# Kernel tuning notes

Hardware: AMD Instinct MI355X
Metric: run time of the kernel (lower is better)

The kernel has to match this reference:

```python
import jax, jax.numpy as jnp
import numpy as np

B, S, D, H, L = 16, 1024, 512, 8, 3
NUM_Q, NUM_C, TOTAL_RES = 10000, 300, 2


def setup_inputs() -> dict:
    k = jax.random.split(jax.random.key(0), 20)
    n = lambda i, s, sc=0.02: jax.random.normal(k[i], s, jnp.float32) * sc
    z = lambda: jnp.zeros((D,), jnp.float32)
    o = lambda: jnp.ones((D,), jnp.float32)
    return {
        'in_ex': jax.random.randint(k[0], (B, S), 0, NUM_Q),
        'in_cat': jax.random.randint(k[1], (B, S), 0, NUM_C),
        'in_res': jax.random.randint(k[2], (B, S), 0, 2),
        'in_pos': n(3, (B, S, D)),
        'en_out': n(4, (B, S, D)),
        'E_res': n(5, (TOTAL_RES + 1, D)),
        'E_ex': n(6, (2 * NUM_Q + 1, D)),
        'E_cat': n(7, (2 * NUM_C + 1, D)),
        'g1': o(), 'be1': z(), 'g2': o(), 'be2': z(), 'g3': o(), 'be3': z(),
        'Wq1': n(8, (D, D)), 'bq1': z(), 'Wk1': n(9, (D, D)), 'bk1': z(),
        'Wv1': n(10, (D, D)), 'bv1': z(), 'Wo1': n(11, (D, D)), 'bo1': z(),
        'Wq2': n(12, (D, D)), 'bq2': z(), 'Wk2': n(13, (D, D)), 'bk2': z(),
        'Wv2': n(14, (D, D)), 'bv2': z(), 'Wo2': n(15, (D, D)), 'bo2': z(),
        'fW1': n(16, (D, D)), 'fb1': z(), 'fW2': n(17, (D, D)), 'fb2': z(),
    }


def layer_norm(x, g, b, eps=1e-5):
    m = x.mean(-1, keepdims=True)
    v = ((x - m) ** 2).mean(-1, keepdims=True)
    return (x - m) / jnp.sqrt(v + eps) * g + b


def pyr_attn(q_in, kv_in, Wq, bq, Wk, bk, Wv, bv, Wo, bo):
    # q_in, kv_in: (S, B, D) as in nn.MultiheadAttention convention
    Sq, Bq, Dm = q_in.shape
    dh = Dm // H
    heads = lambda x: x.reshape(x.shape[0], Bq, H, dh).transpose(1, 2, 0, 3)  # (B,H,S,dh)
    qh = heads(q_in @ Wq + bq)
    kh = heads(kv_in @ Wk + bk)
    vh = heads(kv_in @ Wv + bv)
    Skv = kv_in.shape[0]
    i = jnp.arange(Sq)[:, None]
    Ks, Vs, Ms = [], [], []
    for l in range(L):  # pyramid levels: keys/values avg-pooled by 2**l
        f = 2 ** l
        nb = Skv // f
        Ks.append(kh[:, :, :nb * f].reshape(Bq, H, nb, f, dh).mean(3))
        Vs.append(vh[:, :, :nb * f].reshape(Bq, H, nb, f, dh).mean(3))
        # causal: query i may attend pooled block j only if the block ends at or before i
        Ms.append(i >= (jnp.arange(nb)[None, :] + 1) * f - 1)
    K = jnp.concatenate(Ks, 2)
    V = jnp.concatenate(Vs, 2)
    M = jnp.concatenate(Ms, 1)  # (Sq, K_total) multi-level causal mask
    sc = jnp.einsum('bhqd,bhkd->bhqk', qh, K) / np.sqrt(dh).astype(np.float32)
    sc = jnp.where(M[None, None], sc, -1e9)
    a = jax.nn.softmax(sc, -1)
    out = jnp.einsum('bhqk,bhkd->bhqd', a, V)
    return out.transpose(2, 0, 1, 3).reshape(Sq, Bq, Dm) @ Wo + bo


def reference(in_ex, in_cat, in_res, in_pos, en_out, E_res, E_ex, E_cat,
              g1, be1, g2, be2, g3, be3,
              Wq1, bq1, Wk1, bk1, Wv1, bv1, Wo1, bo1,
              Wq2, bq2, Wk2, bk2, Wv2, bv2, Wo2, bo2,
              fW1, fb1, fW2, fb2):
    # embedding sum (first_block=True)
    out = E_res[in_res] + E_ex[in_ex + NUM_Q * in_res] + E_cat[in_cat + NUM_C * in_res] + in_pos
    out = out.transpose(1, 0, 2)  # (S, B, D)
    out = layer_norm(out, g1, be1)
    out = out + pyr_attn(out, out, Wq1, bq1, Wk1, bk1, Wv1, bv1, Wo1, bo1)
    en = layer_norm(en_out.transpose(1, 0, 2), g2, be2)
    out = out + pyr_attn(out, en, Wq2, bq2, Wk2, bk2, Wv2, bv2, Wo2, bo2)
    out = out.transpose(1, 0, 2)  # (B, S, D)
    out = layer_norm(out, g3, be3)
    out = out + (jax.nn.relu(out @ fW1 + fb1) @ fW2 + fb2)
    return out
```

## Files before the change

kernel.cpp:

```cpp
#include <hip/hip_runtime.h>


#define BB 16
#define SS 1024
#define DD 512
#define HH 8
#define DH 64
#define KTOT 1792
#define NROW (BB*SS)
#define KSW 80

typedef unsigned short u16;
typedef __attribute__((ext_vector_type(8))) u16 u16x8;
typedef __attribute__((ext_vector_type(4))) u16 u16x4;
typedef __attribute__((ext_vector_type(8))) short s16x8;
typedef __attribute__((ext_vector_type(4))) float f32x4;

__device__ __forceinline__ float b2f(u16 u) {
    return __uint_as_float(((unsigned int)u) << 16);
}
__device__ __forceinline__ u16 f2b(float f) {
    unsigned int u = __float_as_uint(f);
    return (u16)((u + 0x7FFF + ((u >> 16) & 1)) >> 16);
}
__device__ __forceinline__ s16x8 u2s8(u16x8 u) {
    union { u16x8 u; s16x8 s; } x; x.u = u; return x.s;
}
__device__ __forceinline__ f32x4 mfma16(s16x8 a, s16x8 b, f32x4 c) {
    return __builtin_amdgcn_mfma_f32_16x16x32_bf16(a, b, c, 0, 0, 0);
}
__device__ __forceinline__ float wave_sum(float v) {
    #pragma unroll
    for (int m = 1; m < 64; m <<= 1) v += __shfl_xor(v, m, 64);
    return v;
}
__device__ __forceinline__ float exp2a(float x) {
    float r;
    asm("v_exp_f32 %0, %1" : "=v"(r) : "v"(x));
    return r;
}
__device__ __forceinline__ unsigned int cvtpk(float a, float b) {
    unsigned int r;
    asm("v_cvt_pk_bf16_f32 %0, %1, %2" : "=v"(r) : "v"(a), "v"(b));
    return r;
}
__device__ __forceinline__ void gl16(const void* g, void* l) {
    __builtin_amdgcn_global_load_lds(
        (const __attribute__((address_space(1))) void*)(unsigned long long)g,
        (__attribute__((address_space(3))) void*)(unsigned int)(unsigned long long)l,
        16, 0, 0);
}

__global__ __launch_bounds__(256) void embed_ln_k(
    const int* __restrict__ in_ex, const int* __restrict__ in_cat,
    const int* __restrict__ in_res, const float* __restrict__ in_pos,
    const float* __restrict__ E_res, const float* __restrict__ E_ex,
    const float* __restrict__ E_cat, const float* __restrict__ g,
    const float* __restrict__ be, float* __restrict__ out)
{
    int wave = threadIdx.x >> 6, lane = threadIdx.x & 63;
    int row = blockIdx.x * 4 + wave;
    int res = in_res[row];
    int ex  = in_ex[row] + 10000 * res;
    int cat = in_cat[row] + 300 * res;
    int d0 = lane * 8;
    const float* pr = &E_res[(size_t)res * DD + d0];
    const float* pe = &E_ex[(size_t)ex * DD + d0];
    const float* pc = &E_cat[(size_t)cat * DD + d0];
    const float* pp = &in_pos[(size_t)row * DD + d0];
    float x[8]; float s = 0.f;
    #pragma unroll
    for (int j = 0; j < 8; j++) { x[j] = pr[j] + pe[j] + pc[j] + pp[j]; s += x[j]; }
    s = wave_sum(s);
    float mean = s * (1.0f / DD);
    float vs = 0.f;
    #pragma unroll
    for (int j = 0; j < 8; j++) { float d = x[j] - mean; vs += d * d; }
    vs = wave_sum(vs);
    float rstd = rsqrtf(vs * (1.0f / DD) + 1e-5f);
    #pragma unroll
    for (int j = 0; j < 8; j++)
        out[(size_t)row * DD + d0 + j] = (x[j] - mean) * rstd * g[d0 + j] + be[d0 + j];
}

template<bool OUTB>
__global__ __launch_bounds__(256) void ln_k(
    const float* __restrict__ x, const float* __restrict__ g,
    const float* __restrict__ be, void* __restrict__ outv)
{
    int wave = threadIdx.x >> 6, lane = threadIdx.x & 63;
    int row = blockIdx.x * 4 + wave;
    int d0 = lane * 8;
    const float* px = &x[(size_t)row * DD + d0];
    float xv[8]; float s = 0.f;
    #pragma unroll
    for (int j = 0; j < 8; j++) { xv[j] = px[j]; s += xv[j]; }
    s = wave_sum(s);
    float mean = s * (1.0f / DD);
    float vs = 0.f;
    #pragma unroll
    for (int j = 0; j < 8; j++) { float d = xv[j] - mean; vs += d * d; }
    vs = wave_sum(vs);
    float rstd = rsqrtf(vs * (1.0f / DD) + 1e-5f);
    #pragma unroll
    for (int j = 0; j < 8; j++) {
        float v = (xv[j] - mean) * rstd * g[d0 + j] + be[d0 + j];
        if (OUTB) ((u16*)outv)[(size_t)row * DD + d0 + j] = f2b(v);
        else      ((float*)outv)[(size_t)row * DD + d0 + j] = v;
    }
}

struct W10 { const float* p[10]; };
__global__ __launch_bounds__(256) void transpose_all_k(W10 wp, u16* __restrict__ dst)
{
    __shared__ __align__(16) u16 T[64 * 72];
    int w = blockIdx.z;
    const float* src = wp.p[w];
    u16* d = dst + (size_t)w * 262144;
    int tk = blockIdx.x;
    int tn = blockIdx.y;
    int tid = threadIdx.x;
    {
        int r = tid >> 4;
        int c4 = (tid & 15) * 4;
        #pragma unroll
        for (int it = 0; it < 4; it++) {
            int kr = it * 16 + r;
            const float* s4 = &src[(size_t)(tk * 64 + kr) * 512 + tn * 64 + c4];
            f32x4 v = *(const f32x4*)s4;
            *(unsigned int*)&T[kr * 72 + c4]     = cvtpk(v[0], v[1]);
            *(unsigned int*)&T[kr * 72 + c4 + 2] = cvtpk(v[2], v[3]);
        }
    }
    __syncthreads();
    {
        int nn = tid >> 2;
        int k16 = (tid & 3) * 16;
        u16x8 a, b;
        #pragma unroll
        for (int j = 0; j < 8; j++) {
            a[j] = T[(k16 + j) * 72 + nn];
            b[j] = T[(k16 + 8 + j) * 72 + nn];
        }
        u16* o = &d[(size_t)(tn * 64 + nn) * 512 + tk * 64 + k16];
        *(u16x8*)&o[0] = a;
        *(u16x8*)&o[8] = b;
    }
}

__global__ __launch_bounds__(256) void pool_vt_k(const u16* __restrict__ Vp, u16* __restrict__ VPt)
{
    __shared__ __align__(16) u16 T[64 * 72];
    int tid = threadIdx.x;
    int st = blockIdx.x;
    int h  = blockIdx.y;
    int b  = blockIdx.z;
    int s0 = st * 64;
    {
        const u16* src = &Vp[((size_t)(b * SS + s0)) * DD + h * DH];
        #pragma unroll
        for (int it = 0; it < 2; it++) {
            int idx = it * 256 + tid;
            int row = idx >> 3, unit = idx & 7;
            *(u16x8*)&T[row * 72 + unit * 8] =
                *(const u16x8*)&src[(size_t)row * DD + unit * 8];
        }
    }
    __syncthreads();
    int d = tid & 63, g = tid >> 6;
    size_t obase = ((size_t)(b * HH + h) * DH + d) * KTOT;
    #pragma unroll
    for (int gg = 0; gg < 2; gg++) {
        int grp = g * 2 + gg;
        u16x8 v;
        #pragma unroll
        for (int j = 0; j < 8; j++) v[j] = T[(grp * 8 + j) * 72 + d];
        *(u16x8*)&VPt[obase + s0 + grp * 8] = v;
    }
    {
        u16x8 v;
        #pragma unroll
        for (int j = 0; j < 8; j++) {
            int sl = g * 8 + j;
            float a = b2f(T[(2 * sl) * 72 + d]) + b2f(T[(2 * sl + 1) * 72 + d]);
            v[j] = f2b(a * 0.5f);
        }
        *(u16x8*)&VPt[obase + 1024 + st * 32 + g * 8] = v;
    }
    {
        u16x4 v;
        #pragma unroll
        for (int j = 0; j < 4; j++) {
            int s2 = g * 4 + j;
            float a = 0.f;
            #pragma unroll
            for (int i = 0; i < 4; i++) a += b2f(T[(4 * s2 + i) * 72 + d]);
            v[j] = f2b(a * 0.25f);
        }
        *(u16x4*)&VPt[obase + 1536 + st * 16 + g * 4] = v;
    }
}

template<bool AF32, bool RELU, bool RES, bool OUTB, bool KLAY>
__global__ __launch_bounds__(256) void gemm_k(
    const void* __restrict__ Av, const u16* __restrict__ Wt,
    const float* __restrict__ bias, const float* __restrict__ resid,
    void* __restrict__ Cv, int M, int K, float oscale)
{
    const int N = 512;
    constexpr int ASW = AF32 ? 40 : 32;
    __shared__ __align__(16) u16 As[2][128 * ASW];
    __shared__ __align__(16) u16 Bs[2][128 * 32];
    int tid = threadIdx.x;
    int wave = tid >> 6, lane = tid & 63;
    int quad = lane >> 4, l16 = lane & 15;
    int m0 = blockIdx.y * 128, n0 = blockIdx.x * 128;
    int wm = (wave >> 1) * 64, wn = (wave & 1) * 64;
    int r = tid >> 1, cg = (tid & 1) * 16;
    int grow = wave * 16 + (lane >> 2);
    int gk = (lane & 3) * 8;
    const float* Af = (const float*)Av;
    const u16*  Ab = (const u16*)Av;
    f32x4 acc[4][4];
    #pragma unroll
    for (int i = 0; i < 4; i++)
        #pragma unroll
        for (int j = 0; j < 4; j++)
            #pragma unroll
            for (int rr = 0; rr < 4; rr++) acc[i][j][rr] = 0.f;

    const int NT = K >> 5;
    f32x4 s0, s1, s2, s3;

    #define ISSUE_B(t, buf) { int k0_ = (t) << 5; \
        gl16(&Wt[(size_t)(n0 + grow) * 512 + k0_ + gk],      &Bs[buf][grow * 32 + gk]); \
        gl16(&Wt[(size_t)(n0 + 64 + grow) * 512 + k0_ + gk], &Bs[buf][(64 + grow) * 32 + gk]); }
    #define ISSUE_A16(t, buf) { int k0_ = (t) << 5; \
        gl16(&Ab[(size_t)(m0 + grow) * K + k0_ + gk],      &As[buf][grow * 32 + gk]); \
        gl16(&Ab[(size_t)(m0 + 64 + grow) * K + k0_ + gk], &As[buf][(64 + grow) * 32 + gk]); }
    #define LOAD_A32(t) { const float* src_ = &Af[(size_t)(m0 + r) * K + ((t) << 5) + cg]; \
        s0 = *(const f32x4*)&src_[0];  s1 = *(const f32x4*)&src_[4]; \
        s2 = *(const f32x4*)&src_[8];  s3 = *(const f32x4*)&src_[12]; }
    #define WRITE_A32(buf) { union { unsigned int w[4]; u16x8 v; } L_, H_; \
        L_.w[0] = cvtpk(s0[0], s0[1]); L_.w[1] = cvtpk(s0[2], s0[3]); \
        L_.w[2] = cvtpk(s1[0], s1[1]); L_.w[3] = cvtpk(s1[2], s1[3]); \
        H_.w[0] = cvtpk(s2[0], s2[1]); H_.w[1] = cvtpk(s2[2], s2[3]); \
        H_.w[2] = cvtpk(s3[0], s3[1]); H_.w[3] = cvtpk(s3[2], s3[3]); \
        *(u16x8*)&As[buf][r * ASW + cg]     = L_.v; \
        *(u16x8*)&As[buf][r * ASW + cg + 8] = H_.v; }

    if (AF32) { LOAD_A32(0); WRITE_A32(0); }
    else      { ISSUE_A16(0, 0); }
    ISSUE_B(0, 0);
    __syncthreads();

    for (int t = 0; t < NT; ++t) {
        int cur = t & 1, nxt = cur ^ 1;
        if (t + 1 < NT) {
            if (AF32) { LOAD_A32(t + 1); }
            else      { ISSUE_A16(t + 1, nxt); }
            ISSUE_B(t + 1, nxt);
        }
        s16x8 af[4], bfr[4];
        #pragma unroll
        for (int i = 0; i < 4; i++)
            af[i] = u2s8(*(const u16x8*)&As[cur][(wm + i * 16 + l16) * ASW + quad * 8]);
        #pragma unroll
        for (int j = 0; j < 4; j++)
            bfr[j] = u2s8(*(const u16x8*)&Bs[cur][(wn + j * 16 + l16) * 32 + quad * 8]);
        #pragma unroll
        for (int i = 0; i < 4; i++)
            #pragma unroll
            for (int j = 0; j < 4; j++)
                acc[i][j] = mfma16(af[i], bfr[j], acc[i][j]);
        if (AF32 && t + 1 < NT) { WRITE_A32(nxt); }
        __syncthreads();
    }
    #undef ISSUE_B
    #undef ISSUE_A16
    #undef LOAD_A32
    #undef WRITE_A32

    #pragma unroll
    for (int j = 0; j < 4; j++) {
        int col = n0 + wn + j * 16 + l16;
        float bv = bias[col];
        #pragma unroll
        for (int i = 0; i < 4; i++) {
            int rowb = m0 + wm + i * 16 + quad * 4;
            if (KLAY) {
                float vv[4];
                #pragma unroll
                for (int rr = 0; rr < 4; rr++) vv[rr] = acc[i][j][rr] + bv;
                int b_ = rowb >> 10, s_ = rowb & 1023;
                size_t bh = (size_t)(b_ * HH + (col >> 6)) * KTOT;
                int dd = col & 63;
                u16* C16 = (u16*)Cv;
                #pragma unroll
                for (int rr = 0; rr < 4; rr++)
                    C16[(bh + s_ + rr) * DH + dd] = f2b(vv[rr]);
                C16[(bh + 1024 + (s_ >> 1)) * DH + dd]     = f2b((vv[0] + vv[1]) * 0.5f);
                C16[(bh + 1024 + (s_ >> 1) + 1) * DH + dd] = f2b((vv[2] + vv[3]) * 0.5f);
                C16[(bh + 1536 + (s_ >> 2)) * DH + dd]     = f2b((vv[0] + vv[1] + vv[2] + vv[3]) * 0.25f);
            } else {
                #pragma unroll
                for (int rr = 0; rr < 4; rr++) {
                    float v = (acc[i][j][rr] + bv) * oscale;
                    if (RELU) v = fmaxf(v, 0.f);
                    int row = rowb + rr;
                    if (RES) v += resid[(size_t)row * N + col];
                    if (OUTB) ((u16*)Cv)[(size_t)row * N + col] = f2b(v);
                    else      ((float*)Cv)[(size_t)row * N + col] = v;
                }
            }
        }
    }
}

__global__ __launch_bounds__(256, 4) void attn_k(
    const u16* __restrict__ Qp, const u16* __restrict__ KP,
    const u16* __restrict__ VPt, u16* __restrict__ Hout)
{
    __shared__ __align__(16) u16 Ksh[2][64 * KSW];
    __shared__ __align__(16) u16 Vsh[2][64 * KSW];
    int tid = threadIdx.x;
    int wave = tid >> 6, lane = tid & 63;
    int quad = lane >> 4, l16 = lane & 15;
    int id = blockIdx.x;
    int h = id & 7;
    int inner = id >> 3;
    int x = inner & 7, b = inner >> 3;

    int wg = x * 4 + wave;
    int tiles[2] = { wg, 63 - wg };

    const u16* Kb = KP  + ((size_t)(b * HH + h)) * KTOT * DH;
    const u16* Vt = VPt + ((size_t)(b * HH + h)) * DH * KTOT;

    s16x8 qa[2][2];
    f32x4 o[2][4];
    float lrun[2];
    int q0a[2];
    #pragma unroll
    for (int c = 0; c < 2; c++) {
        int q0 = tiles[c] * 16;
        q0a[c] = q0;
        lrun[c] = 0.f;
        const u16* qrow = Qp + ((size_t)(b * SS + q0 + l16)) * DD + h * DH;
        qa[c][0] = u2s8(*(const u16x8*)&qrow[quad * 8]);
        qa[c][1] = u2s8(*(const u16x8*)&qrow[32 + quad * 8]);
        #pragma unroll
        for (int j = 0; j < 4; j++)
            #pragma unroll
            for (int rr = 0; rr < 4; rr++) o[c][j][rr] = 0.f;
    }

    int row0 = 8 * (l16 >> 2) + (l16 & 3);

    int u0 = tid, u1 = 256 + tid;
    int kr0 = u0 >> 3, ku0 = (u0 & 7) * 8;
    int kr1 = u1 >> 3, ku1 = (u1 & 7) * 8;

    u16x8 kreg0 = *(const u16x8*)&Kb[(size_t)u0 * 8];
    u16x8 kreg1 = *(const u16x8*)&Kb[(size_t)u1 * 8];
    u16x8 vreg0 = *(const u16x8*)&Vt[(size_t)kr0 * KTOT + ku0];
    u16x8 vreg1 = *(const u16x8*)&Vt[(size_t)kr1 * KTOT + ku1];
    *(u16x8*)&Ksh[0][kr0 * KSW + ku0] = kreg0;
    *(u16x8*)&Ksh[0][kr1 * KSW + ku1] = kreg1;
    *(u16x8*)&Vsh[0][kr0 * KSW + ku0] = vreg0;
    *(u16x8*)&Vsh[0][kr1 * KSW + ku1] = vreg1;
    __syncthreads();

    for (int ch = 0; ch < 28; ch++) {
        int cur = ch & 1;
        int kbase = ch * 64;
        int lv = (ch < 16) ? 0 : (ch < 24) ? 1 : 2;
        if (ch + 1 < 28) {
            int nb = (ch + 1) * 64;
            kreg0 = *(const u16x8*)&Kb[(size_t)nb * DH + u0 * 8];
            kreg1 = *(const u16x8*)&Kb[(size_t)nb * DH + u1 * 8];
            vreg0 = *(const u16x8*)&Vt[(size_t)kr0 * KTOT + nb + ku0];
            vreg1 = *(const u16x8*)&Vt[(size_t)kr1 * KTOT + nb + ku1];
        }

        int efirst = (lv == 0) ? kbase
                   : (lv == 1) ? 2 * (kbase - 1024) + 1
                               : 4 * (kbase - 1536) + 3;
        int elast  = (lv == 0) ? kbase + 63
                   : (lv == 1) ? 2 * (kbase + 63 - 1024) + 1
                               : 4 * (kbase + 63 - 1536) + 3;
        bool act[2];
        #pragma unroll
        for (int c = 0; c < 2; c++) act[c] = (efirst <= q0a[c] + 15);

        if (act[0] | act[1]) {
            s16x8 fA[4], fB[4];
            #pragma unroll
            for (int t = 0; t < 4; t++) {
                const int toff = (t & 1) * 4 + (t >> 1) * 32;
                const u16* kr = &Ksh[cur][(row0 + toff) * KSW];
                fA[t] = u2s8(*(const u16x8*)&kr[quad * 8]);
                fB[t] = u2s8(*(const u16x8*)&kr[32 + quad * 8]);
            }
            s16x8 pfa[2], pfb[2];
            #pragma unroll
            for (int c = 0; c < 2; c++) {
                if (!act[c]) continue;
                f32x4 zt[4];
                __builtin_amdgcn_s_setprio(1);
                #pragma unroll
                for (int t = 0; t < 4; t++) {
                    f32x4 z;
                    #pragma unroll
                    for (int rr = 0; rr < 4; rr++) z[rr] = 0.f;
                    z = mfma16(fA[t], qa[c][0], z);
                    zt[t] = mfma16(fB[t], qa[c][1], z);
                }
                __builtin_amdgcn_s_setprio(0);

                if (elast > q0a[c]) {
                    int q = q0a[c] + l16;
                    int kmaxv = (lv == 0) ? q - kbase
                              : (lv == 1) ? ((q - 1) >> 1) - (kbase - 1024)
                                          : ((q - 3) >> 2) - (kbase - 1536);
                    int thrb = kmaxv - 8 * quad;
                    #pragma unroll
                    for (int t = 0; t < 4; t++) {
                        int thr = thrb - ((t & 1) * 4 + (t >> 1) * 32);
                        #pragma unroll
                        for (int rr = 0; rr < 4; rr++)
                            if (rr > thr) zt[t][rr] = -1e30f;
                    }
                }

                float p[4][4]; float ps0 = 0.f, ps1 = 0.f;
                #pragma unroll
                for (int t = 0; t < 4; t++)
                    #pragma unroll
                    for (int rr = 0; rr < 4; rr++) {
                        p[t][rr] = exp2a(zt[t][rr]);
                        if (t & 1) ps1 += p[t][rr]; else ps0 += p[t][rr];
                    }
                float ps = ps0 + ps1;
                ps += __shfl_xor(ps, 16, 64);
                ps += __shfl_xor(ps, 32, 64);
                lrun[c] += ps;

                union { unsigned int w[4]; u16x8 v; } U0, U1;
                U0.w[0] = cvtpk(p[0][0], p[0][1]); U0.w[1] = cvtpk(p[0][2], p[0][3]);
                U0.w[2] = cvtpk(p[1][0], p[1][1]); U0.w[3] = cvtpk(p[1][2], p[1][3]);
                U1.w[0] = cvtpk(p[2][0], p[2][1]); U1.w[1] = cvtpk(p[2][2], p[2][3]);
                U1.w[2] = cvtpk(p[3][0], p[3][1]); U1.w[3] = cvtpk(p[3][2], p[3][3]);
                pfa[c] = u2s8(U0.v); pfb[c] = u2s8(U1.v);
            }

            s16x8 vA[4], vB[4];
            #pragma unroll
            for (int j = 0; j < 4; j++) {
                const u16* vr = &Vsh[cur][(j * 16 + l16) * KSW];
                vA[j] = u2s8(*(const u16x8*)&vr[quad * 8]);
                vB[j] = u2s8(*(const u16x8*)&vr[32 + quad * 8]);
            }
            __builtin_amdgcn_s_setprio(1);
            #pragma unroll
            for (int c = 0; c < 2; c++) {
                if (!act[c]) continue;
                #pragma unroll
                for (int j = 0; j < 4; j++) {
                    o[c][j] = mfma16(pfa[c], vA[j], o[c][j]);
                    o[c][j] = mfma16(pfb[c], vB[j], o[c][j]);
                }
            }
            __builtin_amdgcn_s_setprio(0);
        }

        if (ch + 1 < 28) {
            int nxt = cur ^ 1;
            *(u16x8*)&Ksh[nxt][kr0 * KSW + ku0] = kreg0;
            *(u16x8*)&Ksh[nxt][kr1 * KSW + ku1] = kreg1;
            *(u16x8*)&Vsh[nxt][kr0 * KSW + ku0] = vreg0;
            *(u16x8*)&Vsh[nxt][kr1 * KSW + ku1] = vreg1;
        }
        __syncthreads();
    }

    #pragma unroll
    for (int c = 0; c < 2; c++) {
        float il = 1.0f / lrun[c];
        float ilr[4];
        #pragma unroll
        for (int rr = 0; rr < 4; rr++) ilr[rr] = __shfl(il, quad * 4 + rr, 64);
        #pragma unroll
        for (int rr = 0; rr < 4; rr++) {
            int q = q0a[c] + quad * 4 + rr;
            #pragma unroll
            for (int j = 0; j < 4; j++)
                Hout[((size_t)(b * SS + q)) * DD + h * DH + j * 16 + l16] = f2b(o[c][j][rr] * ilr[rr]);
        }
    }
}

extern "C" void kernel_launch(void* const* d_in, const int* in_sizes, int n_in,
                              void* d_out, int out_size, void* d_ws, size_t ws_size,
                              hipStream_t stream)
{
    (void)in_sizes; (void)n_in; (void)out_size; (void)ws_size;
    const int* in_ex  = (const int*)d_in[0];
    const int* in_cat = (const int*)d_in[1];
    const int* in_res = (const int*)d_in[2];
    const float* in_pos = (const float*)d_in[3];
    const float* en_out = (const float*)d_in[4];
    const float* E_res  = (const float*)d_in[5];
    const float* E_ex   = (const float*)d_in[6];
    const float* E_cat  = (const float*)d_in[7];
    const float* g1 = (const float*)d_in[8],  *be1 = (const float*)d_in[9];
    const float* g2 = (const float*)d_in[10], *be2 = (const float*)d_in[11];
    const float* g3 = (const float*)d_in[12], *be3 = (const float*)d_in[13];
    const float* Wq1 = (const float*)d_in[14], *bq1 = (const float*)d_in[15];
    const float* Wk1 = (const float*)d_in[16], *bk1 = (const float*)d_in[17];
    const float* Wv1 = (const float*)d_in[18], *bv1 = (const float*)d_in[19];
    const float* Wo1 = (const float*)d_in[20], *bo1 = (const float*)d_in[21];
    const float* Wq2 = (const float*)d_in[22], *bq2 = (const float*)d_in[23];
    const float* Wk2 = (const float*)d_in[24], *bk2 = (const float*)d_in[25];
    const float* Wv2 = (const float*)d_in[26], *bv2 = (const float*)d_in[27];
    const float* Wo2 = (const float*)d_in[28], *bo2 = (const float*)d_in[29];
    const float* fW1 = (const float*)d_in[30], *fb1 = (const float*)d_in[31];
    const float* fW2 = (const float*)d_in[32], *fb2 = (const float*)d_in[33];

    char* ws = (char*)d_ws;
    const size_t U = (size_t)NROW * DD * 2;
    float* x1 = (float*)(ws);
    u16* qb   = (u16*)(ws + 2 * U);
    u16* vb   = (u16*)(ws + 3 * U);
    u16* hb   = (u16*)(ws + 4 * U);
    u16* kp   = (u16*)(ws + 5 * U);
    u16* vpt  = (u16*)(ws + 5 * U + 7 * U / 4);
    u16* wt   = (u16*)(ws + 8 * U + U / 2);
    float* x2 = (float*)d_out;
    u16* en = (u16*)(ws);
    float* x3 = x1;
    float* x4 = (float*)(ws + 5 * U);
    u16* ff1 = hb;

    W10 wp;
    const float* wsrc[10] = {Wq1, Wk1, Wv1, Wo1, Wq2, Wk2, Wv2, Wo2, fW1, fW2};
    for (int i = 0; i < 10; i++) wp.p[i] = wsrc[i];
    transpose_all_k<<<dim3(8, 8, 10), 256, 0, stream>>>(wp, wt);
    u16* tWq1 = wt,            *tWk1 = wt + 262144,   *tWv1 = wt + 2*262144, *tWo1 = wt + 3*262144;
    u16* tWq2 = wt + 4*262144, *tWk2 = wt + 5*262144, *tWv2 = wt + 6*262144, *tWo2 = wt + 7*262144;
    u16* tF1  = wt + 8*262144, *tF2  = wt + 9*262144;

    dim3 ggrid(4, 128);
    dim3 vtgrid(16, 8, 16);
    const float QSC = 0.18033688f;

    embed_ln_k<<<4096, 256, 0, stream>>>(in_ex, in_cat, in_res, in_pos,
                                         E_res, E_ex, E_cat, g1, be1, x1);

    gemm_k<true,false,false,true,false><<<ggrid, 256, 0, stream>>>(x1, tWq1, bq1, nullptr, qb, NROW, 512, QSC);
    gemm_k<true,false,false,true,true ><<<ggrid, 256, 0, stream>>>(x1, tWk1, bk1, nullptr, kp, NROW, 512, 1.0f);
    gemm_k<true,false,false,true,false><<<ggrid, 256, 0, stream>>>(x1, tWv1, bv1, nullptr, vb, NROW, 512, 1.0f);
    pool_vt_k<<<vtgrid, 256, 0, stream>>>(vb, vpt);
    attn_k<<<1024, 256, 0, stream>>>(qb, kp, vpt, hb);
    gemm_k<false,false,true,false,false><<<ggrid, 256, 0, stream>>>(hb, tWo1, bo1, x1, x2, NROW, 512, 1.0f);

    ln_k<true><<<4096, 256, 0, stream>>>(en_out, g2, be2, en);
    gemm_k<true,false,false,true,false><<<ggrid, 256, 0, stream>>>(x2, tWq2, bq2, nullptr, qb, NROW, 512, QSC);
    gemm_k<false,false,false,true,true ><<<ggrid, 256, 0, stream>>>(en, tWk2, bk2, nullptr, kp, NROW, 512, 1.0f);
    gemm_k<false,false,false,true,false><<<ggrid, 256, 0, stream>>>(en, tWv2, bv2, nullptr, vb, NROW, 512, 1.0f);
    pool_vt_k<<<vtgrid, 256, 0, stream>>>(vb, vpt);
    attn_k<<<1024, 256, 0, stream>>>(qb, kp, vpt, hb);
    gemm_k<false,false,true,false,false><<<ggrid, 256, 0, stream>>>(hb, tWo2, bo2, x2, x3, NROW, 512, 1.0f);

    ln_k<false><<<4096, 256, 0, stream>>>(x3, g3, be3, x4);
    gemm_k<true,true,false,true,false><<<ggrid, 256, 0, stream>>>(x4, tF1, fb1, nullptr, ff1, NROW, 512, 1.0f);
    gemm_k<false,false,true,false,false><<<ggrid, 256, 0, stream>>>(ff1, tF2, fb2, x4, (float*)d_out, NROW, 512, 1.0f);
}
```

Baseline: 709.7 us.

## Fuse QKV and KV projection GEMMs into one launch; restructure attention to 8 waves

Adds a fused GEMM kernel that picks one of up to three weight/bias/output sets from blockIdx.x, so the Q/K/V projections (and the cross-attention K/V projections) each run as a single launch sharing the A-matrix stream. Separately, the attention kernel is reworked to use 512 threads with one 16-row query tile per wave instead of two tiles per wave. It also drops the double-buffered shared K/V tiles in favour of a single buffer with two barriers per chunk. This cuts launch count and gives the GPU more concurrent work per launch, at the cost of losing the causal load-balancing tile pairing (wave*8+x gives uneven work across waves) and shared-memory double buffering.

```diff
diff --git a/kernel.cpp b/kernel.cpp
--- a/kernel.cpp
+++ b/kernel.cpp
@@ -276,10 +276,6 @@
         if (AF32 && t + 1 < NT) { WRITE_A32(nxt); }
         __syncthreads();
     }
-    #undef ISSUE_B
-    #undef ISSUE_A16
-    #undef LOAD_A32
-    #undef WRITE_A32
 
     #pragma unroll
     for (int j = 0; j < 4; j++) {
@@ -315,14 +311,148 @@
             }
         }
     }
-}
-
-__global__ __launch_bounds__(256, 4) void attn_k(
+    #undef ISSUE_B
+    #undef ISSUE_A16
+    #undef LOAD_A32
+    #undef WRITE_A32
+}
+
+struct FArgs {
+    const u16* W[3]; const float* bias[3]; void* C[3];
+    float osc[3]; int mode[3];
+};
+template<bool AF32>
+__global__ __launch_bounds__(256) void fused_gemm_k(
+    const void* __restrict__ Av, FArgs fa, int M, int K)
+{
+    constexpr int ASW = AF32 ? 40 : 32;
+    __shared__ __align__(16) u16 As[2][128 * ASW];
+    __shared__ __align__(16) u16 Bs[2][128 * 32];
+    int gsel = blockIdx.x >> 2;
+    int n0 = (blockIdx.x & 3) * 128;
+    const u16* Wt = fa.W[gsel];
+    const float* bias = fa.bias[gsel];
+    void* Cv = fa.C[gsel];
+    float oscale = fa.osc[gsel];
+    int mode = fa.mode[gsel];
+
+    int tid = threadIdx.x;
+    int wave = tid >> 6, lane = tid & 63;
+    int quad = lane >> 4, l16 = lane & 15;
+    int m0 = blockIdx.y * 128;
+    int wm = (wave >> 1) * 64, wn = (wave & 1) * 64;
+    int r = tid >> 1, cg = (tid & 1) * 16;
+    int grow = wave * 16 + (lane >> 2);
+    int gk = (lane & 3) * 8;
+    const float* Af = (const float*)Av;
+    const u16*  Ab = (const u16*)Av;
+    f32x4 acc[4][4];
+    #pragma unroll
+    for (int i = 0; i < 4; i++)
+        #pragma unroll
+        for (int j = 0; j < 4; j++)
+            #pragma unroll
+            for (int rr = 0; rr < 4; rr++) acc[i][j][rr] = 0.f;
+
+    const int NT = K >> 5;
+    f32x4 s0, s1, s2, s3;
+
+    #define ISSUE_B(t, buf) { int k0_ = (t) << 5; \
+        gl16(&Wt[(size_t)(n0 + grow) * 512 + k0_ + gk],      &Bs[buf][grow * 32 + gk]); \
+        gl16(&Wt[(size_t)(n0 + 64 + grow) * 512 + k0_ + gk], &Bs[buf][(64 + grow) * 32 + gk]); }
+    #define ISSUE_A16(t, buf) { int k0_ = (t) << 5; \
+        gl16(&Ab[(size_t)(m0 + grow) * K + k0_ + gk],      &As[buf][grow * 32 + gk]); \
+        gl16(&Ab[(size_t)(m0 + 64 + grow) * K + k0_ + gk], &As[buf][(64 + grow) * 32 + gk]); }
+    #define LOAD_A32(t) { const float* src_ = &Af[(size_t)(m0 + r) * K + ((t) << 5) + cg]; \
+        s0 = *(const f32x4*)&src_[0];  s1 = *(const f32x4*)&src_[4]; \
+        s2 = *(const f32x4*)&src_[8];  s3 = *(const f32x4*)&src_[12]; }
+    #define WRITE_A32(buf) { union { unsigned int w[4]; u16x8 v; } L_, H_; \
+        L_.w[0] = cvtpk(s0[0], s0[1]); L_.w[1] = cvtpk(s0[2], s0[3]); \
+        L_.w[2] = cvtpk(s1[0], s1[1]); L_.w[3] = cvtpk(s1[2], s1[3]); \
+        H_.w[0] = cvtpk(s2[0], s2[1]); H_.w[1] = cvtpk(s2[2], s2[3]); \
+        H_.w[2] = cvtpk(s3[0], s3[1]); H_.w[3] = cvtpk(s3[2], s3[3]); \
+        *(u16x8*)&As[buf][r * ASW + cg]     = L_.v; \
+        *(u16x8*)&As[buf][r * ASW + cg + 8] = H_.v; }
+
+    if (AF32) { LOAD_A32(0); WRITE_A32(0); }
+    else      { ISSUE_A16(0, 0); }
+    ISSUE_B(0, 0);
+    __syncthreads();
+
+    for (int t = 0; t < NT; ++t) {
+        int cur = t & 1, nxt = cur ^ 1;
+        if (t + 1 < NT) {
+            if (AF32) { LOAD_A32(t + 1); }
+            else      { ISSUE_A16(t + 1, nxt); }
+            ISSUE_B(t + 1, nxt);
+        }
+        s16x8 af[4], bfr[4];
+        #pragma unroll
+        for (int i = 0; i < 4; i++)
+            af[i] = u2s8(*(const u16x8*)&As[cur][(wm + i * 16 + l16) * ASW + quad * 8]);
+        #pragma unroll
+        for (int j = 0; j < 4; j++)
+            bfr[j] = u2s8(*(const u16x8*)&Bs[cur][(wn + j * 16 + l16) * 32 + quad * 8]);
+        #pragma unroll
+        for (int i = 0; i < 4; i++)
+            #pragma unroll
+            for (int j = 0; j < 4; j++)
+                acc[i][j] = mfma16(af[i], bfr[j], acc[i][j]);
+        if (AF32 && t + 1 < NT) { WRITE_A32(nxt); }
+        __syncthreads();
+    }
+    #undef ISSUE_B
+    #undef ISSUE_A16
+    #undef LOAD_A32
+    #undef WRITE_A32
+
+    if (mode == 1) {
+        #pragma unroll
+        for (int j = 0; j < 4; j++) {
+            int col = n0 + wn + j * 16 + l16;
+            float bv = bias[col];
+            #pragma unroll
+            for (int i = 0; i < 4; i++) {
+                int rowb = m0 + wm + i * 16 + quad * 4;
+                float vv[4];
+                #pragma unroll
+                for (int rr = 0; rr < 4; rr++) vv[rr] = acc[i][j][rr] + bv;
+                int b_ = rowb >> 10, s_ = rowb & 1023;
+                size_t bh = (size_t)(b_ * HH + (col >> 6)) * KTOT;
+                int dd = col & 63;
+                u16* C16 = (u16*)Cv;
+                #pragma unroll
+                for (int rr = 0; rr < 4; rr++)
+                    C16[(bh + s_ + rr) * DH + dd] = f2b(vv[rr]);
+                C16[(bh + 1024 + (s_ >> 1)) * DH + dd]     = f2b((vv[0] + vv[1]) * 0.5f);
+                C16[(bh + 1024 + (s_ >> 1) + 1) * DH + dd] = f2b((vv[2] + vv[3]) * 0.5f);
+                C16[(bh + 1536 + (s_ >> 2)) * DH + dd]     = f2b((vv[0] + vv[1] + vv[2] + vv[3]) * 0.25f);
+            }
+        }
+    } else {
+        #pragma unroll
+        for (int j = 0; j < 4; j++) {
+            int col = n0 + wn + j * 16 + l16;
+            float bv = bias[col];
+            #pragma unroll
+            for (int i = 0; i < 4; i++) {
+                int rowb = m0 + wm + i * 16 + quad * 4;
+                #pragma unroll
+                for (int rr = 0; rr < 4; rr++) {
+                    float v = (acc[i][j][rr] + bv) * oscale;
+                    ((u16*)Cv)[(size_t)(rowb + rr) * 512 + col] = f2b(v);
+                }
+            }
+        }
+    }
+}
+
+__global__ __launch_bounds__(512) void attn_k(
     const u16* __restrict__ Qp, const u16* __restrict__ KP,
     const u16* __restrict__ VPt, u16* __restrict__ Hout)
 {
-    __shared__ __align__(16) u16 Ksh[2][64 * KSW];
-    __shared__ __align__(16) u16 Vsh[2][64 * KSW];
+    __shared__ __align__(16) u16 Ksh[64 * KSW];
+    __shared__ __align__(16) u16 Vsh[64 * KSW];
     int tid = threadIdx.x;
     int wave = tid >> 6, lane = tid & 63;
     int quad = lane >> 4, l16 = lane & 15;
@@ -331,171 +461,125 @@
     int inner = id >> 3;
     int x = inner & 7, b = inner >> 3;
 
-    int wg = x * 4 + wave;
-    int tiles[2] = { wg, 63 - wg };
+    int tile = wave * 8 + x;
+    int q0 = tile * 16;
 
     const u16* Kb = KP  + ((size_t)(b * HH + h)) * KTOT * DH;
     const u16* Vt = VPt + ((size_t)(b * HH + h)) * DH * KTOT;
 
-    s16x8 qa[2][2];
-    f32x4 o[2][4];
-    float lrun[2];
-    int q0a[2];
-    #pragma unroll
-    for (int c = 0; c < 2; c++) {
-        int q0 = tiles[c] * 16;
-        q0a[c] = q0;
-        lrun[c] = 0.f;
+    s16x8 qa0, qa1;
+    f32x4 o[4];
+    float lrun = 0.f;
+    {
         const u16* qrow = Qp + ((size_t)(b * SS + q0 + l16)) * DD + h * DH;
-        qa[c][0] = u2s8(*(const u16x8*)&qrow[quad * 8]);
-        qa[c][1] = u2s8(*(const u16x8*)&qrow[32 + quad * 8]);
+        qa0 = u2s8(*(const u16x8*)&qrow[quad * 8]);
+        qa1 = u2s8(*(const u16x8*)&qrow[32 + quad * 8]);
         #pragma unroll
         for (int j = 0; j < 4; j++)
             #pragma unroll
-            for (int rr = 0; rr < 4; rr++) o[c][j][rr] = 0.f;
+            for (int rr = 0; rr < 4; rr++) o[j][rr] = 0.f;
     }
 
     int row0 = 8 * (l16 >> 2) + (l16 & 3);
 
-    int u0 = tid, u1 = 256 + tid;
-    int kr0 = u0 >> 3, ku0 = (u0 & 7) * 8;
-    int kr1 = u1 >> 3, ku1 = (u1 & 7) * 8;
-
-    u16x8 kreg0 = *(const u16x8*)&Kb[(size_t)u0 * 8];
-    u16x8 kreg1 = *(const u16x8*)&Kb[(size_t)u1 * 8];
-    u16x8 vreg0 = *(const u16x8*)&Vt[(size_t)kr0 * KTOT + ku0];
-    u16x8 vreg1 = *(const u16x8*)&Vt[(size_t)kr1 * KTOT + ku1];
-    *(u16x8*)&Ksh[0][kr0 * KSW + ku0] = kreg0;
-    *(u16x8*)&Ksh[0][kr1 * KSW + ku1] = kreg1;
-    *(u16x8*)&Vsh[0][kr0 * KSW + ku0] = vreg0;
-    *(u16x8*)&Vsh[0][kr1 * KSW + ku1] = vreg1;
-    __syncthreads();
+    int srow = tid >> 3, sunit = tid & 7;
+    u16x8 kreg = *(const u16x8*)&Kb[(size_t)tid * 8];
+    u16x8 vreg = *(const u16x8*)&Vt[(size_t)srow * KTOT + sunit * 8];
 
     for (int ch = 0; ch < 28; ch++) {
-        int cur = ch & 1;
         int kbase = ch * 64;
         int lv = (ch < 16) ? 0 : (ch < 24) ? 1 : 2;
+        __syncthreads();
+        *(u16x8*)&Ksh[srow * KSW + sunit * 8] = kreg;
+        *(u16x8*)&Vsh[srow * KSW + sunit * 8] = vreg;
+        __syncthreads();
         if (ch + 1 < 28) {
             int nb = (ch + 1) * 64;
-            kreg0 = *(const u16x8*)&Kb[(size_t)nb * DH + u0 * 8];
-            kreg1 = *(const u16x8*)&Kb[(size_t)nb * DH + u1 * 8];
-            vreg0 = *(const u16x8*)&Vt[(size_t)kr0 * KTOT + nb + ku0];
-            vreg1 = *(const u16x8*)&Vt[(size_t)kr1 * KTOT + nb + ku1];
+            kreg = *(const u16x8*)&Kb[(size_t)nb * DH + tid * 8];
+            vreg = *(const u16x8*)&Vt[(size_t)srow * KTOT + nb + sunit * 8];
         }
 
         int efirst = (lv == 0) ? kbase
                    : (lv == 1) ? 2 * (kbase - 1024) + 1
                                : 4 * (kbase - 1536) + 3;
-        int elast  = (lv == 0) ? kbase + 63
-                   : (lv == 1) ? 2 * (kbase + 63 - 1024) + 1
-                               : 4 * (kbase + 63 - 1536) + 3;
-        bool act[2];
-        #pragma unroll
-        for (int c = 0; c < 2; c++) act[c] = (efirst <= q0a[c] + 15);
-
-        if (act[0] | act[1]) {
-            s16x8 fA[4], fB[4];
+        if (efirst > q0 + 15) continue;
+
+        int elast = (lv == 0) ? kbase + 63
+                  : (lv == 1) ? 2 * (kbase + 63 - 1024) + 1
+                              : 4 * (kbase + 63 - 1536) + 3;
+
+        f32x4 zt[4];
+        __builtin_amdgcn_s_setprio(1);
+        #pragma unroll
+        for (int t = 0; t < 4; t++) {
+            const int toff = (t & 1) * 4 + (t >> 1) * 32;
+            const u16* kr = &Ksh[(row0 + toff) * KSW];
+            s16x8 kf0 = u2s8(*(const u16x8*)&kr[quad * 8]);
+            s16x8 kf1 = u2s8(*(const u16x8*)&kr[32 + quad * 8]);
+            f32x4 z;
+            #pragma unroll
+            for (int rr = 0; rr < 4; rr++) z[rr] = 0.f;
+            z = mfma16(kf0, qa0, z);
+            zt[t] = mfma16(kf1, qa1, z);
+        }
+        __builtin_amdgcn_s_setprio(0);
+
+        if (elast > q0) {
+            int q = q0 + l16;
+            int kmaxv = (lv == 0) ? q - kbase
+                      : (lv == 1) ? ((q - 1) >> 1) - (kbase - 1024)
+                                  : ((q - 3) >> 2) - (kbase - 1536);
+            int thrb = kmaxv - 8 * quad;
             #pragma unroll
             for (int t = 0; t < 4; t++) {
-                const int toff = (t & 1) * 4 + (t >> 1) * 32;
-                const u16* kr = &Ksh[cur][(row0 + toff) * KSW];
-                fA[t] = u2s8(*(const u16x8*)&kr[quad * 8]);
-                fB[t] = u2s8(*(const u16x8*)&kr[32 + quad * 8]);
+                int thr = thrb - ((t & 1) * 4 + (t >> 1) * 32);
+                #pragma unroll
+                for (int rr = 0; rr < 4; rr++)
+                    if (rr > thr) zt[t][rr] = -1e30f;
             }
-            s16x8 pfa[2], pfb[2];
-            #pragma unroll
-            for (int c = 0; c < 2; c++) {
-                if (!act[c]) continue;
-                f32x4 zt[4];
-                __builtin_amdgcn_s_setprio(1);
-                #pragma unroll
-                for (int t = 0; t < 4; t++) {
-                    f32x4 z;
-                    #pragma unroll
-                    for (int rr = 0; rr < 4; rr++) z[rr] = 0.f;
-                    z = mfma16(fA[t], qa[c][0], z);
-                    zt[t] = mfma16(fB[t], qa[c][1], z);
-                }
-                __builtin_amdgcn_s_setprio(0);
-
-                if (elast > q0a[c]) {
-                    int q = q0a[c] + l16;
-                    int kmaxv = (lv == 0) ? q - kbase
-                              : (lv == 1) ? ((q - 1) >> 1) - (kbase - 1024)
-                                          : ((q - 3) >> 2) - (kbase - 1536);
-                    int thrb = kmaxv - 8 * quad;
-                    #pragma unroll
-                    for (int t = 0; t < 4; t++) {
-                        int thr = thrb - ((t & 1) * 4 + (t >> 1) * 32);
-                        #pragma unroll
-                        for (int rr = 0; rr < 4; rr++)
-                            if (rr > thr) zt[t][rr] = -1e30f;
-                    }
-                }
-
-                float p[4][4]; float ps0 = 0.f, ps1 = 0.f;
-                #pragma unroll
-                for (int t = 0; t < 4; t++)
-                    #pragma unroll
-                    for (int rr = 0; rr < 4; rr++) {
-                        p[t][rr] = exp2a(zt[t][rr]);
-                        if (t & 1) ps1 += p[t][rr]; else ps0 += p[t][rr];
-                    }
-                float ps = ps0 + ps1;
-                ps += __shfl_xor(ps, 16, 64);
-                ps += __shfl_xor(ps, 32, 64);
-                lrun[c] += ps;
-
-                union { unsigned int w[4]; u16x8 v; } U0, U1;
-                U0.w[0] = cvtpk(p[0][0], p[0][1]); U0.w[1] = cvtpk(p[0][2], p[0][3]);
-                U0.w[2] = cvtpk(p[1][0], p[1][1]); U0.w[3] = cvtpk(p[1][2], p[1][3]);
-                U1.w[0] = cvtpk(p[2][0], p[2][1]); U1.w[1] = cvtpk(p[2][2], p[2][3]);
-                U1.w[2] = cvtpk(p[3][0], p[3][1]); U1.w[3] = cvtpk(p[3][2], p[3][3]);
-                pfa[c] = u2s8(U0.v); pfb[c] = u2s8(U1.v);
+        }
+
+        float p[4][4]; float ps0 = 0.f, ps1 = 0.f;
+        #pragma unroll
+        for (int t = 0; t < 4; t++)
+            #pragma unroll
+            for (int rr = 0; rr < 4; rr++) {
+                p[t][rr] = exp2a(zt[t][rr]);
+                if (t & 1) ps1 += p[t][rr]; else ps0 += p[t][rr];
             }
-
-            s16x8 vA[4], vB[4];
-            #pragma unroll
-            for (int j = 0; j < 4; j++) {
-                const u16* vr = &Vsh[cur][(j * 16 + l16) * KSW];
-                vA[j] = u2s8(*(const u16x8*)&vr[quad * 8]);
-                vB[j] = u2s8(*(const u16x8*)&vr[32 + quad * 8]);
-            }
-            __builtin_amdgcn_s_setprio(1);
-            #pragma unroll
-            for (int c = 0; c < 2; c++) {
-                if (!act[c]) continue;
-                #pragma unroll
-                for (int j = 0; j < 4; j++) {
-                    o[c][j] = mfma16(pfa[c], vA[j], o[c][j]);
-                    o[c][j] = mfma16(pfb[c], vB[j], o[c][j]);
-                }
-            }
-            __builtin_amdgcn_s_setprio(0);
-        }
-
-        if (ch + 1 < 28) {
-            int nxt = cur ^ 1;
-            *(u16x8*)&Ksh[nxt][kr0 * KSW + ku0] = kreg0;
-            *(u16x8*)&Ksh[nxt][kr1 * KSW + ku1] = kreg1;
-            *(u16x8*)&Vsh[nxt][kr0 * KSW + ku0] = vreg0;
-            *(u16x8*)&Vsh[nxt][kr1 * KSW + ku1] = vreg1;
-        }
-        __syncthreads();
-    }
-
-    #pragma unroll
-    for (int c = 0; c < 2; c++) {
-        float il = 1.0f / lrun[c];
+        float ps = ps0 + ps1;
+        ps += __shfl_xor(ps, 16, 64);
+        ps += __shfl_xor(ps, 32, 64);
+        lrun += ps;
+
+        union { unsigned int w[4]; u16x8 v; } U0, U1;
+        U0.w[0] = cvtpk(p[0][0], p[0][1]); U0.w[1] = cvtpk(p[0][2], p[0][3]);
+        U0.w[2] = cvtpk(p[1][0], p[1][1]); U0.w[3] = cvtpk(p[1][2], p[1][3]);
+        U1.w[0] = cvtpk(p[2][0], p[2][1]); U1.w[1] = cvtpk(p[2][2], p[2][3]);
+        U1.w[2] = cvtpk(p[3][0], p[3][1]); U1.w[3] = cvtpk(p[3][2], p[3][3]);
+        s16x8 pf0 = u2s8(U0.v), pf1 = u2s8(U1.v);
+
+        __builtin_amdgcn_s_setprio(1);
+        #pragma unroll
+        for (int j = 0; j < 4; j++) {
+            const u16* vr = &Vsh[(j * 16 + l16) * KSW];
+            o[j] = mfma16(pf0, u2s8(*(const u16x8*)&vr[quad * 8]), o[j]);
+            o[j] = mfma16(pf1, u2s8(*(const u16x8*)&vr[32 + quad * 8]), o[j]);
+        }
+        __builtin_amdgcn_s_setprio(0);
+    }
+
+    {
+        float il = 1.0f / lrun;
         float ilr[4];
         #pragma unroll
         for (int rr = 0; rr < 4; rr++) ilr[rr] = __shfl(il, quad * 4 + rr, 64);
         #pragma unroll
         for (int rr = 0; rr < 4; rr++) {
-            int q = q0a[c] + quad * 4 + rr;
+            int q = q0 + quad * 4 + rr;
             #pragma unroll
             for (int j = 0; j < 4; j++)
-                Hout[((size_t)(b * SS + q)) * DD + h * DH + j * 16 + l16] = f2b(o[c][j][rr] * ilr[rr]);
+                Hout[((size_t)(b * SS + q)) * DD + h * DH + j * 16 + l16] = f2b(o[j][rr] * ilr[rr]);
         }
     }
 }
@@ -557,19 +641,28 @@
     embed_ln_k<<<4096, 256, 0, stream>>>(in_ex, in_cat, in_res, in_pos,
                                          E_res, E_ex, E_cat, g1, be1, x1);
 
-    gemm_k<true,false,false,true,false><<<ggrid, 256, 0, stream>>>(x1, tWq1, bq1, nullptr, qb, NROW, 512, QSC);
-    gemm_k<true,false,false,true,true ><<<ggrid, 256, 0, stream>>>(x1, tWk1, bk1, nullptr, kp, NROW, 512, 1.0f);
-    gemm_k<true,false,false,true,false><<<ggrid, 256, 0, stream>>>(x1, tWv1, bv1, nullptr, vb, NROW, 512, 1.0f);
+    {
+        FArgs fa;
+        fa.W[0] = tWq1; fa.bias[0] = bq1; fa.C[0] = qb; fa.osc[0] = QSC;  fa.mode[0] = 0;
+        fa.W[1] = tWk1; fa.bias[1] = bk1; fa.C[1] = kp; fa.osc[1] = 1.0f; fa.mode[1] = 1;
+        fa.W[2] = tWv1; fa.bias[2] = bv1; fa.C[2] = vb; fa.osc[2] = 1.0f; fa.mode[2] = 0;
+        fused_gemm_k<true><<<dim3(12, 128), 256, 0, stream>>>(x1, fa, NROW, 512);
+    }
     pool_vt_k<<<vtgrid, 256, 0, stream>>>(vb, vpt);
-    attn_k<<<1024, 256, 0, stream>>>(qb, kp, vpt, hb);
+    attn_k<<<1024, 512, 0, stream>>>(qb, kp, vpt, hb);
     gemm_k<false,false,true,false,false><<<ggrid, 256, 0, stream>>>(hb, tWo1, bo1, x1, x2, NROW, 512, 1.0f);
 
     ln_k<true><<<4096, 256, 0, stream>>>(en_out, g2, be2, en);
     gemm_k<true,false,false,true,false><<<ggrid, 256, 0, stream>>>(x2, tWq2, bq2, nullptr, qb, NROW, 512, QSC);
-    gemm_k<false,false,false,true,true ><<<ggrid, 256, 0, stream>>>(en, tWk2, bk2, nullptr, kp, NROW, 512, 1.0f);
-    gemm_k<false,false,false,true,false><<<ggrid, 256, 0, stream>>>(en, tWv2, bv2, nullptr, vb, NROW, 512, 1.0f);
+    {
+        FArgs fa;
+        fa.W[0] = tWk2; fa.bias[0] = bk2; fa.C[0] = kp; fa.osc[0] = 1.0f; fa.mode[0] = 1;
+        fa.W[1] = tWv2; fa.bias[1] = bv2; fa.C[1] = vb; fa.osc[1] = 1.0f; fa.mode[1] = 0;
+        fa.W[2] = nullptr; fa.bias[2] = nullptr; fa.C[2] = nullptr; fa.osc[2] = 1.0f; fa.mode[2] = 0;
+        fused_gemm_k<false><<<dim3(8, 128), 256, 0, stream>>>(en, fa, NROW, 512);
+    }
     pool_vt_k<<<vtgrid, 256, 0, stream>>>(vb, vpt);
-    attn_k<<<1024, 256, 0, stream>>>(qb, kp, vpt, hb);
+    attn_k<<<1024, 512, 0, stream>>>(qb, kp, vpt, hb);
     gemm_k<false,false,true,false,false><<<ggrid, 256, 0, stream>>>(hb, tWo2, bo2, x2, x3, NROW, 512, 1.0f);
 
     ln_k<false><<<4096, 256, 0, stream>>>(x3, g3, be3, x4);
```

New measurement: 601.2 us. 1.18x faster.
